# Performance work log

Measured on AMD Instinct MI355X. Metric: run time of the kernel, lower is better.

The kernel has to match this reference:

```python
import jax, jax.numpy as jnp
import numpy as np
from jax import lax

K = 15            # contrast_kernel
BRIGHT_T = 0.7    # brightness_threshold

def _box_filter(x, k):
    # x: [B,1,H,W]; uniform k x k conv with SAME (zero) padding, matching F.conv2d(padding=k//2)
    kernel = jnp.full((1, 1, k, k), 1.0 / (k * k), dtype=x.dtype)
    pad = k // 2
    return lax.conv_general_dilated(
        x, kernel, window_strides=(1, 1), padding=[(pad, pad), (pad, pad)],
        dimension_numbers=('NCHW', 'OIHW', 'NCHW'))

def _avg_pool_5x5(x):
    # avg_pool2d(kernel=5, stride=1, padding=2), count_include_pad=True (torch default)
    s = lax.reduce_window(x, jnp.array(0.0, x.dtype), lax.add,
                          window_dimensions=(1, 1, 5, 5), window_strides=(1, 1, 1, 1),
                          padding=[(0, 0), (0, 0), (2, 2), (2, 2)])
    return s / jnp.array(25.0, x.dtype)

def setup_inputs() -> dict:
    key = jax.random.key(0)
    img = jax.random.uniform(key, (16, 3, 1024, 1024), dtype=jnp.float32)
    return {"img": img}

def reference(img) -> jnp.ndarray:
    # luminance: [B,1,H,W]
    lum = (0.299 * img[:, 0:1] + 0.587 * img[:, 1:2] + 0.114 * img[:, 2:3])
    brightness_mask = jax.nn.sigmoid((lum - BRIGHT_T) * 10.0)
    local_mean = _box_filter(lum, K)
    local_var = _box_filter((lum - local_mean) ** 2, K)
    contrast_mask = jax.nn.sigmoid(local_var * 50.0 - 0.5)
    max_rgb = jnp.max(img, axis=1, keepdims=True)
    min_rgb = jnp.min(img, axis=1, keepdims=True)
    saturation = (max_rgb - min_rgb) / (max_rgb + 1e-8)
    low_sat_mask = jax.nn.sigmoid((0.3 - saturation) * 10.0)
    combined = jnp.clip(brightness_mask + 0.5 * contrast_mask * low_sat_mask, 0.0, 1.0)
    return _avg_pool_5x5(combined)
```

## Files before the change

### kernel.cpp

```cpp
#include <hip/hip_runtime.h>


#define BLOCK 512
typedef unsigned short u16;
typedef unsigned int u32;

#define SL 104
#define S1 88

__device__ __forceinline__ float blo(u32 u){ return __uint_as_float(u << 16); }
__device__ __forceinline__ float bhi(u32 u){ return __uint_as_float(u & 0xffff0000u); }
__device__ __forceinline__ float bf2f(u16 h){ return __uint_as_float(((u32)h) << 16); }
__device__ __forceinline__ u32 pk2(float lo, float hi){
    u32 r; asm("v_cvt_pk_bf16_f32 %0, %1, %2" : "=v"(r) : "v"(lo), "v"(hi)); return r;
}
__device__ __forceinline__ float sigf(float x){ return 1.f / (1.f + __expf(-x)); }
__device__ __forceinline__ float clamp01(float x){ return fminf(fmaxf(x, 0.f), 1.f); }
__device__ __forceinline__ void unp8(uint4 v, float* o){
    o[0]=blo(v.x); o[1]=bhi(v.x); o[2]=blo(v.y); o[3]=bhi(v.y);
    o[4]=blo(v.z); o[5]=bhi(v.z); o[6]=blo(v.w); o[7]=bhi(v.w);
}
__device__ __forceinline__ float satm(float r_, float g_, float b_){
    float mx = fmaxf(r_, fmaxf(g_, b_));
    float mn = fminf(r_, fminf(g_, b_));
    float sat = (mx - mn) / (mx + 1e-8f);
    return sigf((0.3f - sat) * 10.f);
}

template<bool EDGE>
__device__ __forceinline__ void body(const float* __restrict__ pR,
                                     const float* __restrict__ pG,
                                     const float* __restrict__ pB,
                                     float* __restrict__ po,
                                     int oy, int ox, int tid,
                                     u16* sLum, u16* sT1, u16* sDC)
{
    const float C225 = 1.f / 225.f;
    const float CF   = 50.f / 225.f;

    for (int task = tid; task < 96 * 6; task += BLOCK) {
        int r = task / 6, c = task - r * 6;
        int gy = oy - 16 + r;
        int gxb = ox - 16 + 16 * c;
        u32 pk[8];
        #pragma unroll
        for (int sq = 0; sq < 4; ++sq) {
            int gx = gxb + 4 * sq;
            float l0 = 0.f, l1 = 0.f, l2 = 0.f, l3 = 0.f;
            if (!EDGE || ((unsigned)gy < 1024u && (unsigned)gx < 1024u)) {
                int idx = gy * 1024 + gx;
                float4 R  = *(const float4*)&pR[idx];
                float4 G  = *(const float4*)&pG[idx];
                float4 Bc = *(const float4*)&pB[idx];
                l0 = fmaf(0.299f, R.x, fmaf(0.587f, G.x, 0.114f * Bc.x));
                l1 = fmaf(0.299f, R.y, fmaf(0.587f, G.y, 0.114f * Bc.y));
                l2 = fmaf(0.299f, R.z, fmaf(0.587f, G.z, 0.114f * Bc.z));
                l3 = fmaf(0.299f, R.w, fmaf(0.587f, G.w, 0.114f * Bc.w));
            }
            pk[2 * sq]     = pk2(l0, l1);
            pk[2 * sq + 1] = pk2(l2, l3);
        }
        u16* dst = &sLum[r * SL + 16 * c];
        *(uint4*)dst     = make_uint4(pk[0], pk[1], pk[2], pk[3]);
        *(uint4*)(dst+8) = make_uint4(pk[4], pk[5], pk[6], pk[7]);
    }
    __syncthreads();

    for (int task = tid; task < 96 * 7; task += BLOCK) {
        int r = task / 7, g = task - r * 7;
        int s0 = 12 * g, c0 = s0 & ~7;
        const u16* lr = &sLum[r * SL + c0];
        float lv[32];
        unp8(*(const uint4*)lr,        lv);
        unp8(*(const uint4*)(lr + 8),  lv + 8);
        unp8(*(const uint4*)(lr + 16), lv + 16);
        unp8(*(const uint4*)(lr + 24), lv + 24);
        if (s0 & 4) {
            #pragma unroll
            for (int i = 0; i < 28; ++i) lv[i] = lv[i + 4];
        }
        float o[12];
        float s = 0.f;
        #pragma unroll
        for (int k = 0; k < 15; ++k) s += lv[k];
        o[0] = s;
        #pragma unroll
        for (int j = 1; j < 12; ++j) { s += lv[j + 14] - lv[j - 1]; o[j] = s; }
        u16* dst = &sT1[r * S1 + s0];
        *(uint2*)dst       = make_uint2(pk2(o[0], o[1]),  pk2(o[2], o[3]));
        *(uint2*)(dst + 4) = make_uint2(pk2(o[4], o[5]),  pk2(o[6], o[7]));
        *(uint2*)(dst + 8) = make_uint2(pk2(o[8], o[9]),  pk2(o[10], o[11]));
    }
    __syncthreads();

    for (int task = tid; task < 21 * 21; task += BLOCK) {
        int rg = task / 21, q = task - rg * 21;
        int r0 = 4 * rg;
        const u16* hp = &sT1[r0 * S1 + 4 * q];
        float cs0 = 0.f, cs1 = 0.f, cs2 = 0.f, cs3 = 0.f;
        float a00, a01, a02, a03, a10, a11, a12, a13, a20, a21, a22, a23;
        #pragma unroll
        for (int k = 0; k < 15; ++k) {
            uint2 v = *(const uint2*)(hp + k * S1);
            float x0 = blo(v.x), x1 = bhi(v.x), x2 = blo(v.y), x3 = bhi(v.y);
            if (k == 0) { a00 = x0; a01 = x1; a02 = x2; a03 = x3; }
            if (k == 1) { a10 = x0; a11 = x1; a12 = x2; a13 = x3; }
            if (k == 2) { a20 = x0; a21 = x1; a22 = x2; a23 = x3; }
            cs0 += x0; cs1 += x1; cs2 += x2; cs3 += x3;
        }
        auto emitD = [&](int row) {
            float m0 = cs0 * C225, m1 = cs1 * C225, m2 = cs2 * C225, m3 = cs3 * C225;
            const u16* lp = &sLum[(row + 7) * SL + 4 * q + 4];
            ushort4 A  = *(const ushort4*)lp;
            ushort4 Bv = *(const ushort4*)(lp + 4);
            float t0 = bf2f(A.w)  - m0, t1 = bf2f(Bv.x) - m1;
            float t2 = bf2f(Bv.y) - m2, t3 = bf2f(Bv.z) - m3;
            float d0 = t0 * t0, d1 = t1 * t1, d2 = t2 * t2, d3 = t3 * t3;
            if (EDGE) {
                int gy = oy - 9 + row, gx = ox - 9 + 4 * q;
                bool vy = (unsigned)gy < 1024u;
                d0 = (vy && (unsigned)(gx    ) < 1024u) ? d0 : 0.f;
                d1 = (vy && (unsigned)(gx + 1) < 1024u) ? d1 : 0.f;
                d2 = (vy && (unsigned)(gx + 2) < 1024u) ? d2 : 0.f;
                d3 = (vy && (unsigned)(gx + 3) < 1024u) ? d3 : 0.f;
            }
            *(uint2*)&sDC[row * S1 + 4 * q] = make_uint2(pk2(d0, d1), pk2(d2, d3));
        };
        emitD(r0);
        {
            uint2 v = *(const uint2*)(hp + 15 * S1);
            cs0 += blo(v.x) - a00; cs1 += bhi(v.x) - a01;
            cs2 += blo(v.y) - a02; cs3 += bhi(v.y) - a03;
        }
        emitD(r0 + 1);
        if (r0 + 2 < 82) {
            uint2 v = *(const uint2*)(hp + 16 * S1);
            cs0 += blo(v.x) - a10; cs1 += bhi(v.x) - a11;
            cs2 += blo(v.y) - a12; cs3 += bhi(v.y) - a13;
            emitD(r0 + 2);
            uint2 w = *(const uint2*)(hp + 17 * S1);
            cs0 += blo(w.x) - a20; cs1 += bhi(w.x) - a21;
            cs2 += blo(w.y) - a22; cs3 += bhi(w.y) - a23;
            emitD(r0 + 3);
        }
    }
    __syncthreads();

    for (int task = tid; task < 82 * 6; task += BLOCK) {
        int r = task / 6, g = task - r * 6;
        int s0 = 12 * g, c0 = s0 & ~7;
        const u16* dr = &sDC[r * S1 + c0];
        float lv[32];
        unp8(*(const uint4*)dr,        lv);
        unp8(*(const uint4*)(dr + 8),  lv + 8);
        unp8(*(const uint4*)(dr + 16), lv + 16);
        unp8(*(const uint4*)(dr + 24), lv + 24);
        if (s0 & 4) {
            #pragma unroll
            for (int i = 0; i < 28; ++i) lv[i] = lv[i + 4];
        }
        float o[12];
        float s = 0.f;
        #pragma unroll
        for (int k = 0; k < 15; ++k) s += lv[k];
        o[0] = s;
        #pragma unroll
        for (int j = 1; j < 12; ++j) { s += lv[j + 14] - lv[j - 1]; o[j] = s; }
        u16* dst = &sT1[r * S1 + s0];
        *(uint2*)dst       = make_uint2(pk2(o[0], o[1]),  pk2(o[2], o[3]));
        *(uint2*)(dst + 4) = make_uint2(pk2(o[4], o[5]),  pk2(o[6], o[7]));
        *(uint2*)(dst + 8) = make_uint2(pk2(o[8], o[9]),  pk2(o[10], o[11]));
    }
    __syncthreads();

    for (int task = tid; task < 17 * 17; task += BLOCK) {
        int rg = task / 17, q = task - rg * 17;
        int r0 = 4 * rg;
        const u16* hp = &sT1[r0 * S1 + 4 * q];
        float cs0 = 0.f, cs1 = 0.f, cs2 = 0.f, cs3 = 0.f;
        float a00, a01, a02, a03, a10, a11, a12, a13, a20, a21, a22, a23;
        #pragma unroll
        for (int k = 0; k < 15; ++k) {
            uint2 v = *(const uint2*)(hp + k * S1);
            float x0 = blo(v.x), x1 = bhi(v.x), x2 = blo(v.y), x3 = bhi(v.y);
            if (k == 0) { a00 = x0; a01 = x1; a02 = x2; a03 = x3; }
            if (k == 1) { a10 = x0; a11 = x1; a12 = x2; a13 = x3; }
            if (k == 2) { a20 = x0; a21 = x1; a22 = x2; a23 = x3; }
            cs0 += x0; cs1 += x1; cs2 += x2; cs3 += x3;
        }
        auto emitC = [&](int row) {
            float cm0 = sigf(fmaf(cs0, CF, -0.5f));
            float cm1 = sigf(fmaf(cs1, CF, -0.5f));
            float cm2 = sigf(fmaf(cs2, CF, -0.5f));
            float cm3 = sigf(fmaf(cs3, CF, -0.5f));
            const u16* lp = &sLum[(row + 14) * SL + 4 * q + 12];
            ushort4 A  = *(const ushort4*)lp;
            ushort4 Bv = *(const ushort4*)(lp + 4);
            float bm0 = sigf((bf2f(A.z)  - 0.7f) * 10.f);
            float bm1 = sigf((bf2f(A.w)  - 0.7f) * 10.f);
            float bm2 = sigf((bf2f(Bv.x) - 0.7f) * 10.f);
            float bm3 = sigf((bf2f(Bv.y) - 0.7f) * 10.f);
            int gy = oy - 2 + row, gx0 = ox - 2 + 4 * q;
            int i0 = gy * 1024 + gx0;
            float2 z2 = make_float2(0.f, 0.f);
            float2 Ra, Rb, Ga, Gb, Ba, Bb;
            bool va = true, vb = true;
            if (EDGE) {
                bool vy = (unsigned)gy < 1024u;
                va = vy && (unsigned)gx0 < 1024u;
                vb = vy && (unsigned)(gx0 + 2) < 1024u;
                Ra = va ? *(const float2*)&pR[i0]     : z2;
                Rb = vb ? *(const float2*)&pR[i0 + 2] : z2;
                Ga = va ? *(const float2*)&pG[i0]     : z2;
                Gb = vb ? *(const float2*)&pG[i0 + 2] : z2;
                Ba = va ? *(const float2*)&pB[i0]     : z2;
                Bb = vb ? *(const float2*)&pB[i0 + 2] : z2;
            } else {
                Ra = *(const float2*)&pR[i0];  Rb = *(const float2*)&pR[i0 + 2];
                Ga = *(const float2*)&pG[i0];  Gb = *(const float2*)&pG[i0 + 2];
                Ba = *(const float2*)&pB[i0];  Bb = *(const float2*)&pB[i0 + 2];
            }
            float cb0 = clamp01(bm0 + 0.5f * cm0 * satm(Ra.x, Ga.x, Ba.x));
            float cb1 = clamp01(bm1 + 0.5f * cm1 * satm(Ra.y, Ga.y, Ba.y));
            float cb2 = clamp01(bm2 + 0.5f * cm2 * satm(Rb.x, Gb.x, Bb.x));
            float cb3 = clamp01(bm3 + 0.5f * cm3 * satm(Rb.y, Gb.y, Bb.y));
            if (EDGE) {
                cb0 = va ? cb0 : 0.f;  cb1 = va ? cb1 : 0.f;
                cb2 = vb ? cb2 : 0.f;  cb3 = vb ? cb3 : 0.f;
            }
            *(uint2*)&sDC[row * S1 + 4 * q] = make_uint2(pk2(cb0, cb1), pk2(cb2, cb3));
        };
        emitC(r0);
        {
            uint2 v = *(const uint2*)(hp + 15 * S1);
            cs0 += blo(v.x) - a00; cs1 += bhi(v.x) - a01;
            cs2 += blo(v.y) - a02; cs3 += bhi(v.y) - a03;
        }
        emitC(r0 + 1);
        {
            uint2 v = *(const uint2*)(hp + 16 * S1);
            cs0 += blo(v.x) - a10; cs1 += bhi(v.x) - a11;
            cs2 += blo(v.y) - a12; cs3 += bhi(v.y) - a13;
        }
        emitC(r0 + 2);
        {
            uint2 v = *(const uint2*)(hp + 17 * S1);
            cs0 += blo(v.x) - a20; cs1 += bhi(v.x) - a21;
            cs2 += blo(v.y) - a22; cs3 += bhi(v.y) - a23;
        }
        emitC(r0 + 3);
    }
    __syncthreads();

    for (int task = tid; task < 68 * 4; task += BLOCK) {
        int r = task / 4, g = task & 3;
        int s0 = 16 * g;
        const u16* cr = &sDC[r * S1 + s0];
        float cv[24];
        unp8(*(const uint4*)cr,        cv);
        unp8(*(const uint4*)(cr + 8),  cv + 8);
        unp8(*(const uint4*)(cr + 16), cv + 16);
        float o[16];
        float s = cv[0] + cv[1] + cv[2] + cv[3] + cv[4];
        o[0] = s;
        #pragma unroll
        for (int j = 1; j < 16; ++j) { s += cv[j + 4] - cv[j - 1]; o[j] = s; }
        u16* dst = &sT1[r * S1 + s0];
        *(uint4*)dst = make_uint4(pk2(o[0], o[1]), pk2(o[2], o[3]),
                                  pk2(o[4], o[5]), pk2(o[6], o[7]));
        *(uint4*)(dst + 8) = make_uint4(pk2(o[8],  o[9]),  pk2(o[10], o[11]),
                                        pk2(o[12], o[13]), pk2(o[14], o[15]));
    }
    __syncthreads();

    for (int task = tid; task < 16 * 16; task += BLOCK) {
        int rg = task / 16, q = task & 15;
        int r0 = 4 * rg;
        const u16* hp = &sT1[r0 * S1 + 4 * q];
        float cs0 = 0.f, cs1 = 0.f, cs2 = 0.f, cs3 = 0.f;
        float a00, a01, a02, a03, a10, a11, a12, a13, a20, a21, a22, a23;
        #pragma unroll
        for (int k = 0; k < 5; ++k) {
            uint2 v = *(const uint2*)(hp + k * S1);
            float x0 = blo(v.x), x1 = bhi(v.x), x2 = blo(v.y), x3 = bhi(v.y);
            if (k == 0) { a00 = x0; a01 = x1; a02 = x2; a03 = x3; }
            if (k == 1) { a10 = x0; a11 = x1; a12 = x2; a13 = x3; }
            if (k == 2) { a20 = x0; a21 = x1; a22 = x2; a23 = x3; }
            cs0 += x0; cs1 += x1; cs2 += x2; cs3 += x3;
        }
        const float C25 = 1.f / 25.f;
        float* o0 = po + (size_t)(oy + r0) * 1024 + ox + 4 * q;
        *(float4*)o0 = make_float4(cs0 * C25, cs1 * C25, cs2 * C25, cs3 * C25);
        {
            uint2 v = *(const uint2*)(hp + 5 * S1);
            cs0 += blo(v.x) - a00; cs1 += bhi(v.x) - a01;
            cs2 += blo(v.y) - a02; cs3 += bhi(v.y) - a03;
        }
        *(float4*)(o0 + 1024) = make_float4(cs0 * C25, cs1 * C25, cs2 * C25, cs3 * C25);
        {
            uint2 v = *(const uint2*)(hp + 6 * S1);
            cs0 += blo(v.x) - a10; cs1 += bhi(v.x) - a11;
            cs2 += blo(v.y) - a12; cs3 += bhi(v.y) - a13;
        }
        *(float4*)(o0 + 2048) = make_float4(cs0 * C25, cs1 * C25, cs2 * C25, cs3 * C25);
        {
            uint2 v = *(const uint2*)(hp + 7 * S1);
            cs0 += blo(v.x) - a20; cs1 += bhi(v.x) - a21;
            cs2 += blo(v.y) - a22; cs3 += bhi(v.y) - a23;
        }
        *(float4*)(o0 + 3072) = make_float4(cs0 * C25, cs1 * C25, cs2 * C25, cs3 * C25);
    }
}

__global__ __launch_bounds__(BLOCK, 6)
void wrd_kernel(const float* __restrict__ img, float* __restrict__ out) {
    __shared__ u16 sLum[96 * SL];
    __shared__ u16 sT1[96 * S1];
    __shared__ u16 sDC[82 * S1];

    int bid = blockIdx.x, nwg = gridDim.x;
    int flat = ((nwg & 7) == 0) ? ((bid & 7) * (nwg >> 3) + (bid >> 3)) : bid;
    const int b = flat >> 8;
    const int t = flat & 255;
    const int oy = (t >> 4) * 64, ox = (t & 15) * 64;

    const float* pR = img + (size_t)b * 3145728u;
    const float* pG = pR + 1048576;
    const float* pB = pR + 2097152;
    float* po = out + (size_t)b * 1048576u;

    bool edge = (ox == 0) | (oy == 0) | (ox == 960) | (oy == 960);
    if (edge) body<true >(pR, pG, pB, po, oy, ox, threadIdx.x, sLum, sT1, sDC);
    else      body<false>(pR, pG, pB, po, oy, ox, threadIdx.x, sLum, sT1, sDC);
}

extern "C" void kernel_launch(void* const* d_in, const int* in_sizes, int n_in,
                              void* d_out, int out_size, void* d_ws, size_t ws_size,
                              hipStream_t stream) {
    const float* img = (const float*)d_in[0];
    float* out = (float*)d_out;
    int Bn = in_sizes[0] / (3 * 1024 * 1024);
    int nwg = Bn * 256;
    hipLaunchKernelGGL(wrd_kernel, dim3(nwg), dim3(BLOCK), 0, stream, img, out);
}
```

Baseline: 113.8 us.

## Widen box-filter passes to 16/8-column tasks and use packed f32 adds

The horizontal sliding-sum passes now produce 16 outputs per task instead of 12, which removes the unaligned shift path, and task indexing is reordered column-group-major. The first vertical pass covers 8 columns per task instead of 4. The vertical passes accumulate with v_pk_add_f32 on float pairs and keep negated first rows for the window subtraction. Shared buffers are padded so the wider over-reads and extra rows stay in bounds. The aim is fewer LDS instructions and fewer VALU ops per output, at the cost of more registers per thread and some redundant edge work.

```diff
diff --git a/kernel.cpp b/kernel.cpp
--- a/kernel.cpp
+++ b/kernel.cpp
@@ -4,15 +4,21 @@
 #define BLOCK 512
 typedef unsigned short u16;
 typedef unsigned int u32;
+typedef __attribute__((ext_vector_type(2))) float f32x2;
 
 #define SL 104
 #define S1 88
 
 __device__ __forceinline__ float blo(u32 u){ return __uint_as_float(u << 16); }
 __device__ __forceinline__ float bhi(u32 u){ return __uint_as_float(u & 0xffff0000u); }
-__device__ __forceinline__ float bf2f(u16 h){ return __uint_as_float(((u32)h) << 16); }
 __device__ __forceinline__ u32 pk2(float lo, float hi){
     u32 r; asm("v_cvt_pk_bf16_f32 %0, %1, %2" : "=v"(r) : "v"(lo), "v"(hi)); return r;
+}
+__device__ __forceinline__ f32x2 pka(f32x2 a, f32x2 b){
+    f32x2 d; asm("v_pk_add_f32 %0, %1, %2" : "=v"(d) : "v"(a), "v"(b)); return d;
+}
+__device__ __forceinline__ f32x2 up2(u32 u){
+    f32x2 r; r.x = __uint_as_float(u << 16); r.y = __uint_as_float(u & 0xffff0000u); return r;
 }
 __device__ __forceinline__ float sigf(float x){ return 1.f / (1.f + __expf(-x)); }
 __device__ __forceinline__ float clamp01(float x){ return fminf(fmaxf(x, 0.f), 1.f); }
@@ -66,141 +72,185 @@
     }
     __syncthreads();
 
-    for (int task = tid; task < 96 * 7; task += BLOCK) {
-        int r = task / 7, g = task - r * 7;
-        int s0 = 12 * g, c0 = s0 & ~7;
-        const u16* lr = &sLum[r * SL + c0];
+    for (int task = tid; task < 6 * 96; task += BLOCK) {
+        int g = task / 96, r = task - g * 96;
+        int s0 = 16 * g;
+        const u16* lr = &sLum[r * SL + s0];
         float lv[32];
         unp8(*(const uint4*)lr,        lv);
         unp8(*(const uint4*)(lr + 8),  lv + 8);
         unp8(*(const uint4*)(lr + 16), lv + 16);
         unp8(*(const uint4*)(lr + 24), lv + 24);
-        if (s0 & 4) {
-            #pragma unroll
-            for (int i = 0; i < 28; ++i) lv[i] = lv[i + 4];
-        }
-        float o[12];
+        float o[16];
         float s = 0.f;
         #pragma unroll
         for (int k = 0; k < 15; ++k) s += lv[k];
         o[0] = s;
         #pragma unroll
-        for (int j = 1; j < 12; ++j) { s += lv[j + 14] - lv[j - 1]; o[j] = s; }
+        for (int j = 1; j < 16; ++j) { s += lv[j + 14] - lv[j - 1]; o[j] = s; }
         u16* dst = &sT1[r * S1 + s0];
-        *(uint2*)dst       = make_uint2(pk2(o[0], o[1]),  pk2(o[2], o[3]));
-        *(uint2*)(dst + 4) = make_uint2(pk2(o[4], o[5]),  pk2(o[6], o[7]));
-        *(uint2*)(dst + 8) = make_uint2(pk2(o[8], o[9]),  pk2(o[10], o[11]));
-    }
-    __syncthreads();
-
-    for (int task = tid; task < 21 * 21; task += BLOCK) {
-        int rg = task / 21, q = task - rg * 21;
-        int r0 = 4 * rg;
-        const u16* hp = &sT1[r0 * S1 + 4 * q];
-        float cs0 = 0.f, cs1 = 0.f, cs2 = 0.f, cs3 = 0.f;
-        float a00, a01, a02, a03, a10, a11, a12, a13, a20, a21, a22, a23;
-        #pragma unroll
-        for (int k = 0; k < 15; ++k) {
-            uint2 v = *(const uint2*)(hp + k * S1);
-            float x0 = blo(v.x), x1 = bhi(v.x), x2 = blo(v.y), x3 = bhi(v.y);
-            if (k == 0) { a00 = x0; a01 = x1; a02 = x2; a03 = x3; }
-            if (k == 1) { a10 = x0; a11 = x1; a12 = x2; a13 = x3; }
-            if (k == 2) { a20 = x0; a21 = x1; a22 = x2; a23 = x3; }
-            cs0 += x0; cs1 += x1; cs2 += x2; cs3 += x3;
+        if (g < 5) {
+            *(uint4*)dst     = make_uint4(pk2(o[0],o[1]), pk2(o[2],o[3]),
+                                          pk2(o[4],o[5]), pk2(o[6],o[7]));
+            *(uint4*)(dst+8) = make_uint4(pk2(o[8],o[9]),  pk2(o[10],o[11]),
+                                          pk2(o[12],o[13]),pk2(o[14],o[15]));
+        } else {
+            *(uint2*)dst = make_uint2(pk2(o[0],o[1]), pk2(o[2],o[3]));
+        }
+    }
+    __syncthreads();
+
+    for (int task = tid; task < 231; task += BLOCK) {
+        int rg = task / 11, cg = task - rg * 11;
+        int r0 = 4 * rg, c0 = 8 * cg;
+        const u16* hp = &sT1[r0 * S1 + c0];
+        f32x2 cs0, cs1, cs2, cs3;
+        f32x2 n00,n01,n02,n03, n10,n11,n12,n13, n20,n21,n22,n23;
+        {
+            uint4 v = *(const uint4*)hp;
+            cs0 = up2(v.x); cs1 = up2(v.y); cs2 = up2(v.z); cs3 = up2(v.w);
+            n00 = -cs0; n01 = -cs1; n02 = -cs2; n03 = -cs3;
+        }
+        {
+            uint4 v = *(const uint4*)(hp + S1);
+            f32x2 e0 = up2(v.x), e1 = up2(v.y), e2 = up2(v.z), e3 = up2(v.w);
+            n10 = -e0; n11 = -e1; n12 = -e2; n13 = -e3;
+            cs0 = pka(cs0, e0); cs1 = pka(cs1, e1);
+            cs2 = pka(cs2, e2); cs3 = pka(cs3, e3);
+        }
+        {
+            uint4 v = *(const uint4*)(hp + 2 * S1);
+            f32x2 e0 = up2(v.x), e1 = up2(v.y), e2 = up2(v.z), e3 = up2(v.w);
+            n20 = -e0; n21 = -e1; n22 = -e2; n23 = -e3;
+            cs0 = pka(cs0, e0); cs1 = pka(cs1, e1);
+            cs2 = pka(cs2, e2); cs3 = pka(cs3, e3);
+        }
+        #pragma unroll
+        for (int k = 3; k < 15; ++k) {
+            uint4 v = *(const uint4*)(hp + k * S1);
+            cs0 = pka(cs0, up2(v.x)); cs1 = pka(cs1, up2(v.y));
+            cs2 = pka(cs2, up2(v.z)); cs3 = pka(cs3, up2(v.w));
         }
         auto emitD = [&](int row) {
-            float m0 = cs0 * C225, m1 = cs1 * C225, m2 = cs2 * C225, m3 = cs3 * C225;
-            const u16* lp = &sLum[(row + 7) * SL + 4 * q + 4];
-            ushort4 A  = *(const ushort4*)lp;
-            ushort4 Bv = *(const ushort4*)(lp + 4);
-            float t0 = bf2f(A.w)  - m0, t1 = bf2f(Bv.x) - m1;
-            float t2 = bf2f(Bv.y) - m2, t3 = bf2f(Bv.z) - m3;
-            float d0 = t0 * t0, d1 = t1 * t1, d2 = t2 * t2, d3 = t3 * t3;
+            const u16* lrow = &sLum[(row + 7) * SL + c0];
+            u32 aw  = *(const u32*)(lrow + 6);
+            uint4 bv = *(const uint4*)(lrow + 8);
+            float L0 = bhi(aw);
+            float L1 = blo(bv.x), L2 = bhi(bv.x);
+            float L3 = blo(bv.y), L4 = bhi(bv.y);
+            float L5 = blo(bv.z), L6 = bhi(bv.z);
+            float L7 = blo(bv.w);
+            float t0 = fmaf(-C225, cs0.x, L0), t1 = fmaf(-C225, cs0.y, L1);
+            float t2 = fmaf(-C225, cs1.x, L2), t3 = fmaf(-C225, cs1.y, L3);
+            float t4 = fmaf(-C225, cs2.x, L4), t5 = fmaf(-C225, cs2.y, L5);
+            float t6 = fmaf(-C225, cs3.x, L6), t7 = fmaf(-C225, cs3.y, L7);
+            float d0=t0*t0, d1=t1*t1, d2=t2*t2, d3=t3*t3;
+            float d4=t4*t4, d5=t5*t5, d6=t6*t6, d7=t7*t7;
             if (EDGE) {
-                int gy = oy - 9 + row, gx = ox - 9 + 4 * q;
+                int gy = oy - 9 + row, gx = ox - 9 + c0;
                 bool vy = (unsigned)gy < 1024u;
                 d0 = (vy && (unsigned)(gx    ) < 1024u) ? d0 : 0.f;
                 d1 = (vy && (unsigned)(gx + 1) < 1024u) ? d1 : 0.f;
                 d2 = (vy && (unsigned)(gx + 2) < 1024u) ? d2 : 0.f;
                 d3 = (vy && (unsigned)(gx + 3) < 1024u) ? d3 : 0.f;
+                d4 = (vy && (unsigned)(gx + 4) < 1024u) ? d4 : 0.f;
+                d5 = (vy && (unsigned)(gx + 5) < 1024u) ? d5 : 0.f;
+                d6 = (vy && (unsigned)(gx + 6) < 1024u) ? d6 : 0.f;
+                d7 = (vy && (unsigned)(gx + 7) < 1024u) ? d7 : 0.f;
             }
-            *(uint2*)&sDC[row * S1 + 4 * q] = make_uint2(pk2(d0, d1), pk2(d2, d3));
+            *(uint4*)&sDC[row * S1 + c0] =
+                make_uint4(pk2(d0,d1), pk2(d2,d3), pk2(d4,d5), pk2(d6,d7));
         };
         emitD(r0);
         {
-            uint2 v = *(const uint2*)(hp + 15 * S1);
-            cs0 += blo(v.x) - a00; cs1 += bhi(v.x) - a01;
-            cs2 += blo(v.y) - a02; cs3 += bhi(v.y) - a03;
+            uint4 v = *(const uint4*)(hp + 15 * S1);
+            cs0 = pka(pka(cs0, up2(v.x)), n00); cs1 = pka(pka(cs1, up2(v.y)), n01);
+            cs2 = pka(pka(cs2, up2(v.z)), n02); cs3 = pka(pka(cs3, up2(v.w)), n03);
         }
         emitD(r0 + 1);
-        if (r0 + 2 < 82) {
-            uint2 v = *(const uint2*)(hp + 16 * S1);
-            cs0 += blo(v.x) - a10; cs1 += bhi(v.x) - a11;
-            cs2 += blo(v.y) - a12; cs3 += bhi(v.y) - a13;
-            emitD(r0 + 2);
-            uint2 w = *(const uint2*)(hp + 17 * S1);
-            cs0 += blo(w.x) - a20; cs1 += bhi(w.x) - a21;
-            cs2 += blo(w.y) - a22; cs3 += bhi(w.y) - a23;
-            emitD(r0 + 3);
-        }
-    }
-    __syncthreads();
-
-    for (int task = tid; task < 82 * 6; task += BLOCK) {
-        int r = task / 6, g = task - r * 6;
-        int s0 = 12 * g, c0 = s0 & ~7;
-        const u16* dr = &sDC[r * S1 + c0];
+        {
+            uint4 v = *(const uint4*)(hp + 16 * S1);
+            cs0 = pka(pka(cs0, up2(v.x)), n10); cs1 = pka(pka(cs1, up2(v.y)), n11);
+            cs2 = pka(pka(cs2, up2(v.z)), n12); cs3 = pka(pka(cs3, up2(v.w)), n13);
+        }
+        emitD(r0 + 2);
+        {
+            uint4 v = *(const uint4*)(hp + 17 * S1);
+            cs0 = pka(pka(cs0, up2(v.x)), n20); cs1 = pka(pka(cs1, up2(v.y)), n21);
+            cs2 = pka(pka(cs2, up2(v.z)), n22); cs3 = pka(pka(cs3, up2(v.w)), n23);
+        }
+        emitD(r0 + 3);
+    }
+    __syncthreads();
+
+    for (int task = tid; task < 5 * 82; task += BLOCK) {
+        int g = task / 82, r = task - g * 82;
+        int s0 = 16 * g;
+        const u16* dr = &sDC[r * S1 + s0];
         float lv[32];
         unp8(*(const uint4*)dr,        lv);
         unp8(*(const uint4*)(dr + 8),  lv + 8);
         unp8(*(const uint4*)(dr + 16), lv + 16);
         unp8(*(const uint4*)(dr + 24), lv + 24);
-        if (s0 & 4) {
-            #pragma unroll
-            for (int i = 0; i < 28; ++i) lv[i] = lv[i + 4];
-        }
-        float o[12];
+        float o[16];
         float s = 0.f;
         #pragma unroll
         for (int k = 0; k < 15; ++k) s += lv[k];
         o[0] = s;
         #pragma unroll
-        for (int j = 1; j < 12; ++j) { s += lv[j + 14] - lv[j - 1]; o[j] = s; }
+        for (int j = 1; j < 16; ++j) { s += lv[j + 14] - lv[j - 1]; o[j] = s; }
         u16* dst = &sT1[r * S1 + s0];
-        *(uint2*)dst       = make_uint2(pk2(o[0], o[1]),  pk2(o[2], o[3]));
-        *(uint2*)(dst + 4) = make_uint2(pk2(o[4], o[5]),  pk2(o[6], o[7]));
-        *(uint2*)(dst + 8) = make_uint2(pk2(o[8], o[9]),  pk2(o[10], o[11]));
-    }
-    __syncthreads();
-
-    for (int task = tid; task < 17 * 17; task += BLOCK) {
+        if (g < 4) {
+            *(uint4*)dst     = make_uint4(pk2(o[0],o[1]), pk2(o[2],o[3]),
+                                          pk2(o[4],o[5]), pk2(o[6],o[7]));
+            *(uint4*)(dst+8) = make_uint4(pk2(o[8],o[9]),  pk2(o[10],o[11]),
+                                          pk2(o[12],o[13]),pk2(o[14],o[15]));
+        } else {
+            *(uint2*)dst = make_uint2(pk2(o[0],o[1]), pk2(o[2],o[3]));
+        }
+    }
+    __syncthreads();
+
+    for (int task = tid; task < 289; task += BLOCK) {
         int rg = task / 17, q = task - rg * 17;
-        int r0 = 4 * rg;
-        const u16* hp = &sT1[r0 * S1 + 4 * q];
-        float cs0 = 0.f, cs1 = 0.f, cs2 = 0.f, cs3 = 0.f;
-        float a00, a01, a02, a03, a10, a11, a12, a13, a20, a21, a22, a23;
-        #pragma unroll
-        for (int k = 0; k < 15; ++k) {
+        int r0 = 4 * rg, c0 = 4 * q;
+        const u16* hp = &sT1[r0 * S1 + c0];
+        f32x2 cs0, cs1, n00,n01, n10,n11, n20,n21;
+        {
+            uint2 v = *(const uint2*)hp;
+            cs0 = up2(v.x); cs1 = up2(v.y);
+            n00 = -cs0; n01 = -cs1;
+        }
+        {
+            uint2 v = *(const uint2*)(hp + S1);
+            f32x2 e0 = up2(v.x), e1 = up2(v.y);
+            n10 = -e0; n11 = -e1;
+            cs0 = pka(cs0, e0); cs1 = pka(cs1, e1);
+        }
+        {
+            uint2 v = *(const uint2*)(hp + 2 * S1);
+            f32x2 e0 = up2(v.x), e1 = up2(v.y);
+            n20 = -e0; n21 = -e1;
+            cs0 = pka(cs0, e0); cs1 = pka(cs1, e1);
+        }
+        #pragma unroll
+        for (int k = 3; k < 15; ++k) {
             uint2 v = *(const uint2*)(hp + k * S1);
-            float x0 = blo(v.x), x1 = bhi(v.x), x2 = blo(v.y), x3 = bhi(v.y);
-            if (k == 0) { a00 = x0; a01 = x1; a02 = x2; a03 = x3; }
-            if (k == 1) { a10 = x0; a11 = x1; a12 = x2; a13 = x3; }
-            if (k == 2) { a20 = x0; a21 = x1; a22 = x2; a23 = x3; }
-            cs0 += x0; cs1 += x1; cs2 += x2; cs3 += x3;
+            cs0 = pka(cs0, up2(v.x)); cs1 = pka(cs1, up2(v.y));
         }
         auto emitC = [&](int row) {
-            float cm0 = sigf(fmaf(cs0, CF, -0.5f));
-            float cm1 = sigf(fmaf(cs1, CF, -0.5f));
-            float cm2 = sigf(fmaf(cs2, CF, -0.5f));
-            float cm3 = sigf(fmaf(cs3, CF, -0.5f));
-            const u16* lp = &sLum[(row + 14) * SL + 4 * q + 12];
-            ushort4 A  = *(const ushort4*)lp;
-            ushort4 Bv = *(const ushort4*)(lp + 4);
-            float bm0 = sigf((bf2f(A.z)  - 0.7f) * 10.f);
-            float bm1 = sigf((bf2f(A.w)  - 0.7f) * 10.f);
-            float bm2 = sigf((bf2f(Bv.x) - 0.7f) * 10.f);
-            float bm3 = sigf((bf2f(Bv.y) - 0.7f) * 10.f);
-            int gy = oy - 2 + row, gx0 = ox - 2 + 4 * q;
+            float cm0 = sigf(fmaf(cs0.x, CF, -0.5f));
+            float cm1 = sigf(fmaf(cs0.y, CF, -0.5f));
+            float cm2 = sigf(fmaf(cs1.x, CF, -0.5f));
+            float cm3 = sigf(fmaf(cs1.y, CF, -0.5f));
+            const u16* lr = &sLum[(row + 14) * SL + c0 + 14];
+            u32 la = *(const u32*)lr;
+            u32 lb = *(const u32*)(lr + 2);
+            float bm0 = sigf((blo(la) - 0.7f) * 10.f);
+            float bm1 = sigf((bhi(la) - 0.7f) * 10.f);
+            float bm2 = sigf((blo(lb) - 0.7f) * 10.f);
+            float bm3 = sigf((bhi(lb) - 0.7f) * 10.f);
+            int gy = oy - 2 + row, gx0 = ox - 2 + c0;
             int i0 = gy * 1024 + gx0;
             float2 z2 = make_float2(0.f, 0.f);
             float2 Ra, Rb, Ga, Gb, Ba, Bb;
@@ -228,32 +278,29 @@
                 cb0 = va ? cb0 : 0.f;  cb1 = va ? cb1 : 0.f;
                 cb2 = vb ? cb2 : 0.f;  cb3 = vb ? cb3 : 0.f;
             }
-            *(uint2*)&sDC[row * S1 + 4 * q] = make_uint2(pk2(cb0, cb1), pk2(cb2, cb3));
+            *(uint2*)&sDC[row * S1 + c0] = make_uint2(pk2(cb0,cb1), pk2(cb2,cb3));
         };
         emitC(r0);
         {
             uint2 v = *(const uint2*)(hp + 15 * S1);
-            cs0 += blo(v.x) - a00; cs1 += bhi(v.x) - a01;
-            cs2 += blo(v.y) - a02; cs3 += bhi(v.y) - a03;
+            cs0 = pka(pka(cs0, up2(v.x)), n00); cs1 = pka(pka(cs1, up2(v.y)), n01);
         }
         emitC(r0 + 1);
         {
             uint2 v = *(const uint2*)(hp + 16 * S1);
-            cs0 += blo(v.x) - a10; cs1 += bhi(v.x) - a11;
-            cs2 += blo(v.y) - a12; cs3 += bhi(v.y) - a13;
+            cs0 = pka(pka(cs0, up2(v.x)), n10); cs1 = pka(pka(cs1, up2(v.y)), n11);
         }
         emitC(r0 + 2);
         {
             uint2 v = *(const uint2*)(hp + 17 * S1);
-            cs0 += blo(v.x) - a20; cs1 += bhi(v.x) - a21;
-            cs2 += blo(v.y) - a22; cs3 += bhi(v.y) - a23;
+            cs0 = pka(pka(cs0, up2(v.x)), n20); cs1 = pka(pka(cs1, up2(v.y)), n21);
         }
         emitC(r0 + 3);
     }
     __syncthreads();
 
-    for (int task = tid; task < 68 * 4; task += BLOCK) {
-        int r = task / 4, g = task & 3;
+    for (int task = tid; task < 4 * 68; task += BLOCK) {
+        int g = task / 68, r = task - g * 68;
         int s0 = 16 * g;
         const u16* cr = &sDC[r * S1 + s0];
         float cv[24];
@@ -273,50 +320,62 @@
     }
     __syncthreads();
 
-    for (int task = tid; task < 16 * 16; task += BLOCK) {
-        int rg = task / 16, q = task & 15;
-        int r0 = 4 * rg;
-        const u16* hp = &sT1[r0 * S1 + 4 * q];
-        float cs0 = 0.f, cs1 = 0.f, cs2 = 0.f, cs3 = 0.f;
-        float a00, a01, a02, a03, a10, a11, a12, a13, a20, a21, a22, a23;
-        #pragma unroll
-        for (int k = 0; k < 5; ++k) {
-            uint2 v = *(const uint2*)(hp + k * S1);
-            float x0 = blo(v.x), x1 = bhi(v.x), x2 = blo(v.y), x3 = bhi(v.y);
-            if (k == 0) { a00 = x0; a01 = x1; a02 = x2; a03 = x3; }
-            if (k == 1) { a10 = x0; a11 = x1; a12 = x2; a13 = x3; }
-            if (k == 2) { a20 = x0; a21 = x1; a22 = x2; a23 = x3; }
-            cs0 += x0; cs1 += x1; cs2 += x2; cs3 += x3;
+    for (int task = tid; task < 256; task += BLOCK) {
+        int rg = task >> 4, q = task & 15;
+        int r0 = 4 * rg, c0 = 4 * q;
+        const u16* hp = &sT1[r0 * S1 + c0];
+        f32x2 cs0, cs1, n00,n01, n10,n11, n20,n21;
+        {
+            uint2 v = *(const uint2*)hp;
+            cs0 = up2(v.x); cs1 = up2(v.y);
+            n00 = -cs0; n01 = -cs1;
+        }
+        {
+            uint2 v = *(const uint2*)(hp + S1);
+            f32x2 e0 = up2(v.x), e1 = up2(v.y);
+            n10 = -e0; n11 = -e1;
+            cs0 = pka(cs0, e0); cs1 = pka(cs1, e1);
+        }
+        {
+            uint2 v = *(const uint2*)(hp + 2 * S1);
+            f32x2 e0 = up2(v.x), e1 = up2(v.y);
+            n20 = -e0; n21 = -e1;
+            cs0 = pka(cs0, e0); cs1 = pka(cs1, e1);
+        }
+        {
+            uint2 v = *(const uint2*)(hp + 3 * S1);
+            cs0 = pka(cs0, up2(v.x)); cs1 = pka(cs1, up2(v.y));
+        }
+        {
+            uint2 v = *(const uint2*)(hp + 4 * S1);
+            cs0 = pka(cs0, up2(v.x)); cs1 = pka(cs1, up2(v.y));
         }
         const float C25 = 1.f / 25.f;
-        float* o0 = po + (size_t)(oy + r0) * 1024 + ox + 4 * q;
-        *(float4*)o0 = make_float4(cs0 * C25, cs1 * C25, cs2 * C25, cs3 * C25);
+        float* o0 = po + (size_t)(oy + r0) * 1024 + ox + c0;
+        *(float4*)o0 = make_float4(cs0.x*C25, cs0.y*C25, cs1.x*C25, cs1.y*C25);
         {
             uint2 v = *(const uint2*)(hp + 5 * S1);
-            cs0 += blo(v.x) - a00; cs1 += bhi(v.x) - a01;
-            cs2 += blo(v.y) - a02; cs3 += bhi(v.y) - a03;
-        }
-        *(float4*)(o0 + 1024) = make_float4(cs0 * C25, cs1 * C25, cs2 * C25, cs3 * C25);
+            cs0 = pka(pka(cs0, up2(v.x)), n00); cs1 = pka(pka(cs1, up2(v.y)), n01);
+        }
+        *(float4*)(o0 + 1024) = make_float4(cs0.x*C25, cs0.y*C25, cs1.x*C25, cs1.y*C25);
         {
             uint2 v = *(const uint2*)(hp + 6 * S1);
-            cs0 += blo(v.x) - a10; cs1 += bhi(v.x) - a11;
-            cs2 += blo(v.y) - a12; cs3 += bhi(v.y) - a13;
-        }
-        *(float4*)(o0 + 2048) = make_float4(cs0 * C25, cs1 * C25, cs2 * C25, cs3 * C25);
+            cs0 = pka(pka(cs0, up2(v.x)), n10); cs1 = pka(pka(cs1, up2(v.y)), n11);
+        }
+        *(float4*)(o0 + 2048) = make_float4(cs0.x*C25, cs0.y*C25, cs1.x*C25, cs1.y*C25);
         {
             uint2 v = *(const uint2*)(hp + 7 * S1);
-            cs0 += blo(v.x) - a20; cs1 += bhi(v.x) - a21;
-            cs2 += blo(v.y) - a22; cs3 += bhi(v.y) - a23;
-        }
-        *(float4*)(o0 + 3072) = make_float4(cs0 * C25, cs1 * C25, cs2 * C25, cs3 * C25);
+            cs0 = pka(pka(cs0, up2(v.x)), n20); cs1 = pka(pka(cs1, up2(v.y)), n21);
+        }
+        *(float4*)(o0 + 3072) = make_float4(cs0.x*C25, cs0.y*C25, cs1.x*C25, cs1.y*C25);
     }
 }
 
 __global__ __launch_bounds__(BLOCK, 6)
 void wrd_kernel(const float* __restrict__ img, float* __restrict__ out) {
-    __shared__ u16 sLum[96 * SL];
-    __shared__ u16 sT1[96 * S1];
-    __shared__ u16 sDC[82 * S1];
+    __shared__ u16 sLum[96 * SL + 16];
+    __shared__ u16 sT1[98 * S1];
+    __shared__ u16 sDC[84 * S1 + 16];
 
     int bid = blockIdx.x, nwg = gridDim.x;
     int flat = ((nwg & 7) == 0) ? ((bid & 7) * (nwg >> 3) + (bid >> 3)) : bid;
```

Result: slower. 116.1 us (+2.1%).
